# Kernel optimization log

Hardware: AMD Instinct MI355X
Metric: run time of the kernel (lower is better)

Reference implementation:

```python
import jax, jax.numpy as jnp
import numpy as np

T, B, E = 2048, 2, 1024
H = 16
D = E // H


def setup_inputs() -> dict:
    key = jax.random.key(0)
    ks = jax.random.split(key, 7)
    s = 1.0 / np.sqrt(E)
    return {
        "query": jax.random.normal(ks[0], (T, B, E), jnp.float32),
        "key": jax.random.normal(ks[1], (T, B, E), jnp.float32),
        "value": jax.random.normal(ks[2], (T, B, E), jnp.float32),
        "in_proj_weight": jax.random.normal(ks[3], (3 * E, E), jnp.float32) * s,
        "in_proj_bias": jax.random.normal(ks[4], (3 * E,), jnp.float32) * 0.02,
        "out_proj_weight": jax.random.normal(ks[5], (E, E), jnp.float32) * s,
        "out_proj_bias": jax.random.normal(ks[6], (E,), jnp.float32) * 0.02,
    }


def reference(query, key, value, in_proj_weight, in_proj_bias, out_proj_weight, out_proj_bias):
    tgt_len, bsz, embed_dim = query.shape
    src_len = key.shape[0]
    head_dim = embed_dim // H
    # packed in-projection (F.linear: x @ W.T + b)
    w_q, w_k, w_v = jnp.split(in_proj_weight, 3, axis=0)
    b_q, b_k, b_v = jnp.split(in_proj_bias, 3, axis=0)
    q = query @ w_q.T + b_q   # [T, B, E]
    k = key @ w_k.T + b_k     # [S, B, E]
    v = value @ w_v.T + b_v   # [S, B, E]
    # [T,B,E] -> [B,H,T,D]
    q = q.reshape(tgt_len, bsz, H, head_dim).transpose(1, 2, 0, 3)
    k = k.reshape(src_len, bsz, H, head_dim).transpose(1, 2, 0, 3)
    v = v.reshape(src_len, bsz, H, head_dim).transpose(1, 2, 0, 3)
    scale = 1.0 / jnp.sqrt(jnp.asarray(head_dim, q.dtype))
    scores = jnp.einsum("bhtd,bhsd->bhts", q, k) * scale  # [B,H,T,S]
    attn_weights = jax.nn.softmax(scores, axis=-1)
    attn = jnp.einsum("bhts,bhsd->bhtd", attn_weights, v)  # [B,H,T,D]
    # [B,H,T,D] -> [T,B,E]
    attn = attn.transpose(2, 0, 1, 3).reshape(tgt_len, bsz, embed_dim)
    attn_output = attn @ out_proj_weight.T + out_proj_bias  # [T,B,E]
    # averaged attention weights over heads (average_attn_weights=True)
    avg_weights = jnp.sum(attn_weights, axis=1) / H  # [B,T,S]
    return attn_output, avg_weights
```

## Files before the change

### kernel.cpp

```cpp
#include <hip/hip_runtime.h>
#include <hip/hip_bf16.h>

typedef float  f32x2  __attribute__((ext_vector_type(2)));
typedef float  f32x4  __attribute__((ext_vector_type(4)));
typedef float  f32x16 __attribute__((ext_vector_type(16)));
typedef __bf16 bf16x8 __attribute__((ext_vector_type(8)));

#define MFMA16(A,B,C) __builtin_amdgcn_mfma_f32_16x16x32_bf16((A),(B),(C),0,0,0)
#define MFMA32(A,B,C) __builtin_amdgcn_mfma_f32_32x32x16_bf16((A),(B),(C),0,0,0)
#define EXP2(x) __builtin_amdgcn_exp2f(x)
#define LOG2(x) __builtin_amdgcn_logf(x)

static constexpr int Tn = 2048, Bn = 2, En = 1024, Hn = 16, Dn = 64;
static constexpr float kQScale = 0.125f * 1.4426950408889634f;

static __device__ __forceinline__ unsigned pack2(float a, float b) {
  union { __bf16 h[2]; unsigned u; } un;
  un.h[0] = (__bf16)a; un.h[1] = (__bf16)b;
  return un.u;
}

static __device__ __forceinline__ void gload_lds16(const void* g, void* l) {
  __builtin_amdgcn_global_load_lds(
      (const __attribute__((address_space(1))) void*)g,
      (__attribute__((address_space(3))) void*)l, 16, 0, 0);
}

__global__ __launch_bounds__(256)
void k_cvt(const float* __restrict__ q, const float* __restrict__ k,
           const float* __restrict__ v, const float* __restrict__ w3,
           const float* __restrict__ wo,
           __bf16* __restrict__ qb, __bf16* __restrict__ kb,
           __bf16* __restrict__ vb, __bf16* __restrict__ w3b,
           __bf16* __restrict__ wob)
{
  const size_t g = (size_t)blockIdx.x * 256 + threadIdx.x;
  const float* src;
  __bf16* dst;
  size_t off;
  if (g < 524288)        { src = q;  dst = qb;  off = g; }
  else if (g < 1048576)  { src = k;  dst = kb;  off = g - 524288; }
  else if (g < 1572864)  { src = v;  dst = vb;  off = g - 1048576; }
  else if (g < 1966080)  { src = w3; dst = w3b; off = g - 1572864; }
  else                   { src = wo; dst = wob; off = g - 1966080; }
  const float* p = src + off * 8;
  f32x4 a = *reinterpret_cast<const f32x4*>(p);
  f32x4 b = *reinterpret_cast<const f32x4*>(p + 4);
  bf16x8 o;
  #pragma unroll
  for (int e = 0; e < 4; ++e) { o[e] = (__bf16)a[e]; o[e + 4] = (__bf16)b[e]; }
  *reinterpret_cast<bf16x8*>(dst + off * 8) = o;
}

__global__ __launch_bounds__(256)
void k_qkv(const __bf16* __restrict__ Xq, const __bf16* __restrict__ Xk,
           const __bf16* __restrict__ Xv, const __bf16* __restrict__ W,
           const float* __restrict__ bias,
           __bf16* __restrict__ q_ws, __bf16* __restrict__ k_ws,
           __bf16* __restrict__ v_ws)
{
  __shared__ __align__(16) char a_lds[2][8192];
  __shared__ __align__(16) char b_lds[2][8192];
  const int tid = threadIdx.x;
  const int lane = tid & 63, w = tid >> 6;
  const int wr = w >> 1, wc = w & 1;
  const int ag = lane >> 4, lr = lane & 15;
  const int mBase = blockIdx.x * 128;
  const int oBase = blockIdx.y * 128;
  const int which = blockIdx.y >> 3;
  const __bf16* X  = (which == 0) ? Xq : ((which == 1) ? Xk : Xv);
  const __bf16* Wt = W + (size_t)oBase * En;
  __bf16* dst = (which == 0) ? q_ws : ((which == 1) ? k_ws : v_ws);
  const float oscale = (which == 0) ? kQScale : 1.0f;

  const int gA = w;
  const __bf16* pa0 = X  + (size_t)(mBase + lane) * En + gA * 8;
  const __bf16* pa1 = X  + (size_t)(mBase + 64 + lane) * En + gA * 8;
  const __bf16* pb0 = Wt + (size_t)(lane) * En + gA * 8;
  const __bf16* pb1 = Wt + (size_t)(64 + lane) * En + gA * 8;

  f32x4 acc[4][4];
  #pragma unroll
  for (int i = 0; i < 4; ++i)
    #pragma unroll
    for (int j = 0; j < 4; ++j) { f32x4 z = {0.f, 0.f, 0.f, 0.f}; acc[i][j] = z; }

  gload_lds16(pa0, &a_lds[0][gA * 2048]);
  gload_lds16(pa1, &a_lds[0][gA * 2048 + 1024]);
  gload_lds16(pb0, &b_lds[0][gA * 2048]);
  gload_lds16(pb1, &b_lds[0][gA * 2048 + 1024]);
  __syncthreads();

  for (int kt = 0; kt < 32; ++kt) {
    const int cur = kt & 1, nxt = cur ^ 1;
    if (kt + 1 < 32) {
      const int kk = (kt + 1) * 32;
      gload_lds16(pa0 + kk, &a_lds[nxt][gA * 2048]);
      gload_lds16(pa1 + kk, &a_lds[nxt][gA * 2048 + 1024]);
      gload_lds16(pb0 + kk, &b_lds[nxt][gA * 2048]);
      gload_lds16(pb1 + kk, &b_lds[nxt][gA * 2048 + 1024]);
    }
    bf16x8 af[4], bfr[4];
    #pragma unroll
    for (int mb = 0; mb < 4; ++mb)
      af[mb] = *(const bf16x8*)(&a_lds[cur][ag * 2048 + (wr * 64 + mb * 16 + lr) * 16]);
    #pragma unroll
    for (int nb = 0; nb < 4; ++nb)
      bfr[nb] = *(const bf16x8*)(&b_lds[cur][ag * 2048 + (wc * 64 + nb * 16 + lr) * 16]);
    #pragma unroll
    for (int mb = 0; mb < 4; ++mb)
      #pragma unroll
      for (int nb = 0; nb < 4; ++nb)
        acc[mb][nb] = MFMA16(af[mb], bfr[nb], acc[mb][nb]);
    __syncthreads();
  }

  #pragma unroll
  for (int nb = 0; nb < 4; ++nb) {
    int oG = oBase + wc * 64 + nb * 16 + lr;
    float bv = bias[oG];
    int oS = oG & (En - 1);
    int h = oS >> 6, d = oS & 63;
    #pragma unroll
    for (int mb = 0; mb < 4; ++mb)
      #pragma unroll
      for (int r = 0; r < 4; ++r) {
        int i = mBase + wr * 64 + mb * 16 + ag * 4 + r;
        int t = i >> 1, b2 = i & 1;
        dst[(((size_t)(b2 * Hn + h)) * Tn + t) * Dn + d] =
            (__bf16)((acc[mb][nb][r] + bv) * oscale);
      }
  }
}

__global__ __launch_bounds__(256)
void k_transpose_v(const __bf16* __restrict__ v_ws, __bf16* __restrict__ vt_ws)
{
  __shared__ __bf16 tile[64][72];
  const int bh = blockIdx.x >> 5;
  const int tt = blockIdx.x & 31;
  const int tid = threadIdx.x;
  const __bf16* src = v_ws + ((size_t)bh * Tn + tt * 64) * Dn;
  #pragma unroll
  for (int it = 0; it < 2; ++it) {
    int gi = tid + it * 256;
    int row = gi >> 3, gg = gi & 7;
    *reinterpret_cast<bf16x8*>(&tile[row][gg * 8]) =
        *reinterpret_cast<const bf16x8*>(src + row * Dn + gg * 8);
  }
  __syncthreads();
  __bf16* dst = vt_ws + (size_t)bh * Dn * Tn + tt * 64;
  #pragma unroll
  for (int it = 0; it < 2; ++it) {
    int gi = tid + it * 256;
    int drow = gi >> 3, tg = gi & 7;
    bf16x8 vv;
    #pragma unroll
    for (int e = 0; e < 8; ++e) vv[e] = tile[tg * 8 + e][drow];
    *reinterpret_cast<bf16x8*>(dst + (size_t)drow * Tn + tg * 8) = vv;
  }
}

__global__ __launch_bounds__(256, 2)
void k_flash(const __bf16* __restrict__ q_ws, const __bf16* __restrict__ k_ws,
             const __bf16* __restrict__ vt_ws, __bf16* __restrict__ ctx,
             float* __restrict__ adj_g)
{
  __shared__ __align__(16) char kv_sm[2 * 16384];

  const int tid = threadIdx.x;
  const int lane = tid & 63, w = tid >> 6;
  const int tl = lane & 31, hi = lane >> 5;
  const int bh = blockIdx.x >> 4;
  const int qt = blockIdx.x & 15;
  const int t0w = qt * 128 + w * 32;

  const __bf16* kbase  = k_ws + (size_t)bh * Tn * Dn;
  const __bf16* vtbase = vt_ws + (size_t)bh * Dn * Tn;

  bf16x8 qf[4];
  {
    const __bf16* qrow = q_ws + ((size_t)bh * Tn + t0w + tl) * Dn + hi * 8;
    #pragma unroll
    for (int c = 0; c < 4; ++c)
      qf[c] = *reinterpret_cast<const bf16x8*>(qrow + c * 16);
  }

  union { unsigned u[4]; bf16x8 v; } onu;
  #pragma unroll
  for (int j = 0; j < 4; ++j) onu.u[j] = 0x3F803F80u;
  const bf16x8 kOne = onu.v;

  f32x16 accO0, accO1, accL;
  #pragma unroll
  for (int i = 0; i < 16; ++i) { accO0[i] = 0.f; accO1[i] = 0.f; accL[i] = 0.f; }
  float m_run = -INFINITY;

  const int r0 = tid >> 3, s0 = tid & 7;
  const int ldso = ((s0 ^ (r0 & 7)) << 4);
  const int ko0 = r0 * 128 + ldso;

  bf16x8 rk0 = *(const bf16x8*)(kbase + r0 * 64 + s0 * 8);
  bf16x8 rk1 = *(const bf16x8*)(kbase + (r0 + 32) * 64 + s0 * 8);
  bf16x8 rv0 = *(const bf16x8*)(vtbase + (size_t)r0 * Tn + s0 * 8);
  bf16x8 rv1 = *(const bf16x8*)(vtbase + (size_t)(r0 + 32) * Tn + s0 * 8);
  *(bf16x8*)(kv_sm + ko0) = rk0;
  *(bf16x8*)(kv_sm + ko0 + 4096) = rk1;
  *(bf16x8*)(kv_sm + 8192 + ko0) = rv0;
  *(bf16x8*)(kv_sm + 8192 + ko0 + 4096) = rv1;

  for (int st = 0; st < 32; ++st) {
    __syncthreads();
    const char* cur = kv_sm + (st & 1) * 16384;
    char* nxt = kv_sm + ((st + 1) & 1) * 16384;
    if (st + 1 < 32) {
      const __bf16* kn = kbase + (size_t)(st + 1) * 64 * Dn;
      const __bf16* vn = vtbase + (st + 1) * 64;
      rk0 = *(const bf16x8*)(kn + r0 * 64 + s0 * 8);
      rk1 = *(const bf16x8*)(kn + (r0 + 32) * 64 + s0 * 8);
      rv0 = *(const bf16x8*)(vn + (size_t)r0 * Tn + s0 * 8);
      rv1 = *(const bf16x8*)(vn + (size_t)(r0 + 32) * Tn + s0 * 8);
    }

    f32x16 sc0, sc1;
    #pragma unroll
    for (int i = 0; i < 16; ++i) { sc0[i] = 0.f; sc1[i] = 0.f; }
    const char* kr0 = cur + tl * 128;
    const char* kr1 = cur + (32 + tl) * 128;
    __builtin_amdgcn_s_setprio(1);
    #pragma unroll
    for (int c = 0; c < 4; ++c) {
      const int off = (((2 * c + hi) ^ (tl & 7)) << 4);
      sc0 = MFMA32(*(const bf16x8*)(kr0 + off), qf[c], sc0);
      sc1 = MFMA32(*(const bf16x8*)(kr1 + off), qf[c], sc1);
    }
    __builtin_amdgcn_s_setprio(0);

    float mx[8];
    #pragma unroll
    for (int i = 0; i < 8; ++i)
      mx[i] = fmaxf(fmaxf(sc0[i], sc0[i + 8]), fmaxf(sc1[i], sc1[i + 8]));
    float tm = fmaxf(fmaxf(fmaxf(mx[0], mx[1]), fmaxf(mx[2], mx[3])),
                     fmaxf(fmaxf(mx[4], mx[5]), fmaxf(mx[6], mx[7])));
    tm = fmaxf(tm, __shfl_xor(tm, 32, 64));
    if (__any(tm > m_run + 8.0f)) {
      const float mn = fmaxf(m_run, tm);
      const float es = EXP2(m_run - mn);
      m_run = mn;
      #pragma unroll
      for (int q = 0; q < 4; ++q)
        #pragma unroll
        for (int rr = 0; rr < 4; ++rr) {
          const float e = __shfl(es, 8 * q + 4 * hi + rr, 32);
          accO0[q * 4 + rr] *= e;
          accO1[q * 4 + rr] *= e;
          accL[q * 4 + rr] *= e;
        }
    }
    #pragma unroll
    for (int i = 0; i < 16; ++i) {
      sc0[i] = EXP2(sc0[i] - m_run);
      sc1[i] = EXP2(sc1[i] - m_run);
    }

    unsigned wA0[4], wB0[4], wA1[4], wB1[4];
    #pragma unroll
    for (int g = 0; g < 4; ++g) {
      wA0[g] = pack2(sc0[4 * g],     sc0[4 * g + 1]);
      wB0[g] = pack2(sc0[4 * g + 2], sc0[4 * g + 3]);
      wA1[g] = pack2(sc1[4 * g],     sc1[4 * g + 1]);
      wB1[g] = pack2(sc1[4 * g + 2], sc1[4 * g + 3]);
    }
    bf16x8 pa[2][2];
    #pragma unroll
    for (int sb = 0; sb < 2; ++sb) {
      const unsigned* WA = sb ? wA1 : wA0;
      const unsigned* WB = sb ? wB1 : wB0;
      #pragma unroll
      for (int c = 0; c < 2; ++c) {
        unsigned w0 = WA[2 * c], w2 = WA[2 * c + 1];
        unsigned w1 = WB[2 * c], w3 = WB[2 * c + 1];
        asm("v_permlane32_swap_b32 %0, %1" : "+v"(w0), "+v"(w2));
        asm("v_permlane32_swap_b32 %0, %1" : "+v"(w1), "+v"(w3));
        union { unsigned u[4]; bf16x8 v; } uu;
        uu.u[0] = w0; uu.u[1] = w1; uu.u[2] = w2; uu.u[3] = w3;
        pa[sb][c] = uu.v;
      }
    }

    const char* vr0 = cur + 8192 + tl * 128;
    const char* vr1 = cur + 8192 + (32 + tl) * 128;
    __builtin_amdgcn_s_setprio(1);
    #pragma unroll
    for (int sb = 0; sb < 2; ++sb)
      #pragma unroll
      for (int c = 0; c < 2; ++c) {
        const int off = (((sb * 4 + c * 2 + hi) ^ (tl & 7)) << 4);
        accO0 = MFMA32(pa[sb][c], *(const bf16x8*)(vr0 + off), accO0);
        accO1 = MFMA32(pa[sb][c], *(const bf16x8*)(vr1 + off), accO1);
        accL  = MFMA32(pa[sb][c], kOne, accL);
      }
    __builtin_amdgcn_s_setprio(0);

    if (st + 1 < 32) {
      *(bf16x8*)(nxt + ko0) = rk0;
      *(bf16x8*)(nxt + ko0 + 4096) = rk1;
      *(bf16x8*)(nxt + 8192 + ko0) = rv0;
      *(bf16x8*)(nxt + 8192 + ko0 + 4096) = rv1;
    }
  }

  const int b2 = bh >> 4, h = bh & 15;
  float adjv[16];
  #pragma unroll
  for (int q = 0; q < 4; ++q)
    #pragma unroll
    for (int rr = 0; rr < 4; ++rr) {
      const int j = q * 4 + rr;
      const float lv = 1.0f / accL[j];
      const int t = t0w + 8 * q + 4 * hi + rr;
      __bf16* cp = ctx + ((size_t)t * Bn + b2) * En + h * 64 + tl;
      cp[0]  = (__bf16)(accO0[j] * lv);
      cp[32] = (__bf16)(accO1[j] * lv);
      const float mrow = __shfl(m_run, 8 * q + 4 * hi + rr, 32);
      adjv[j] = mrow + LOG2(16.0f * accL[j]);
    }
  if (tl == 0) {
    #pragma unroll
    for (int q = 0; q < 4; ++q)
      #pragma unroll
      for (int rr = 0; rr < 4; ++rr) {
        const int t = t0w + 8 * q + 4 * hi + rr;
        adj_g[(size_t)bh * Tn + t] = adjv[q * 4 + rr];
      }
  }
}

__global__ __launch_bounds__(256)
void k_avgw(const __bf16* __restrict__ q_ws, const __bf16* __restrict__ k_ws,
            const float* __restrict__ adj_g, float* __restrict__ avg_out)
{
  __shared__ __align__(16) char q_sm[2][8192];
  __shared__ __align__(16) char k_sm[2][8192];
  __shared__ __align__(16) float adj_sm[16][64];

  const int tid = threadIdx.x;
  const int lane = tid & 63, w = tid >> 6;
  const int tl = lane & 31, hi = lane >> 5;
  const int b2 = blockIdx.x >> 10;
  const int tt = (blockIdx.x >> 5) & 31;
  const int ss = blockIdx.x & 31;
  const int thalf = (w >> 1) * 32, shalf = (w & 1) * 32;

  #pragma unroll
  for (int it = 0; it < 4; ++it) {
    int idx = tid + it * 256;
    int h = idx >> 6, trow = idx & 63;
    adj_sm[h][trow] = adj_g[((size_t)(b2 * Hn + h)) * Tn + tt * 64 + trow];
  }

  const size_t hstride = (size_t)Tn * Dn;
  const __bf16* qb = q_ws + ((size_t)(b2 * Hn) * Tn + tt * 64) * Dn;
  const __bf16* kb = k_ws + ((size_t)(b2 * Hn) * Tn + ss * 64) * Dn;

  const int r0 = tid >> 3, s0 = tid & 7;
  const int ldso = ((s0 ^ (r0 & 7)) << 4);
  const int ko0 = r0 * 128 + ldso;

  bf16x8 rq0 = *(const bf16x8*)(qb + r0 * 64 + s0 * 8);
  bf16x8 rq1 = *(const bf16x8*)(qb + (r0 + 32) * 64 + s0 * 8);
  bf16x8 rk0 = *(const bf16x8*)(kb + r0 * 64 + s0 * 8);
  bf16x8 rk1 = *(const bf16x8*)(kb + (r0 + 32) * 64 + s0 * 8);
  *(bf16x8*)(q_sm[0] + ko0) = rq0;
  *(bf16x8*)(q_sm[0] + ko0 + 4096) = rq1;
  *(bf16x8*)(k_sm[0] + ko0) = rk0;
  *(bf16x8*)(k_sm[0] + ko0 + 4096) = rk1;

  f32x16 avg;
  #pragma unroll
  for (int i = 0; i < 16; ++i) avg[i] = 0.f;

  for (int h = 0; h < Hn; ++h) {
    __syncthreads();
    const char* qc = q_sm[h & 1];
    const char* kc = k_sm[h & 1];
    char* qn = q_sm[(h + 1) & 1];
    char* kn = k_sm[(h + 1) & 1];
    if (h + 1 < Hn) {
      const __bf16* qp = qb + (size_t)(h + 1) * hstride;
      const __bf16* kp = kb + (size_t)(h + 1) * hstride;
      rq0 = *(const bf16x8*)(qp + r0 * 64 + s0 * 8);
      rq1 = *(const bf16x8*)(qp + (r0 + 32) * 64 + s0 * 8);
      rk0 = *(const bf16x8*)(kp + r0 * 64 + s0 * 8);
      rk1 = *(const bf16x8*)(kp + (r0 + 32) * 64 + s0 * 8);
    }

    f32x16 sc;
    #pragma unroll
    for (int i = 0; i < 16; ++i) sc[i] = 0.f;
    const char* qr = qc + (thalf + tl) * 128;
    const char* kr = kc + (shalf + tl) * 128;
    #pragma unroll
    for (int c = 0; c < 4; ++c) {
      const int off = (((2 * c + hi) ^ (tl & 7)) << 4);
      sc = MFMA32(*(const bf16x8*)(qr + off), *(const bf16x8*)(kr + off), sc);
    }

    #pragma unroll
    for (int q = 0; q < 4; ++q) {
      f32x4 ad = *(const f32x4*)&adj_sm[h][thalf + 8 * q + 4 * hi];
      #pragma unroll
      for (int r = 0; r < 4; ++r)
        avg[q * 4 + r] += EXP2(sc[q * 4 + r] - ad[r]);
    }

    if (h + 1 < Hn) {
      *(bf16x8*)(qn + ko0) = rq0;
      *(bf16x8*)(qn + ko0 + 4096) = rq1;
      *(bf16x8*)(kn + ko0) = rk0;
      *(bf16x8*)(kn + ko0 + 4096) = rk1;
    }
  }

  #pragma unroll
  for (int q = 0; q < 4; ++q)
    #pragma unroll
    for (int r = 0; r < 4; ++r) {
      int t = tt * 64 + thalf + 8 * q + 4 * hi + r;
      int s = ss * 64 + shalf + tl;
      avg_out[((size_t)(b2 * Tn + t)) * Tn + s] = avg[q * 4 + r];
    }
}

__global__ __launch_bounds__(256)
void k_outproj(const __bf16* __restrict__ ctx, const __bf16* __restrict__ W,
               const float* __restrict__ bias, float* __restrict__ out)
{
  __shared__ __align__(16) char a_lds[2][8192];
  __shared__ __align__(16) char b_lds[2][8192];
  const int tid = threadIdx.x;
  const int lane = tid & 63, w = tid >> 6;
  const int wr = w >> 1, wc = w & 1;
  const int ag = lane >> 4, lr = lane & 15;
  const int mBase = blockIdx.x * 128;
  const int oBase = blockIdx.y * 128;
  const __bf16* Wt = W + (size_t)oBase * En;

  const int gA = w;
  const __bf16* pa0 = ctx + (size_t)(mBase + lane) * En + gA * 8;
  const __bf16* pa1 = ctx + (size_t)(mBase + 64 + lane) * En + gA * 8;
  const __bf16* pb0 = Wt + (size_t)(lane) * En + gA * 8;
  const __bf16* pb1 = Wt + (size_t)(64 + lane) * En + gA * 8;

  f32x4 acc[4][4];
  #pragma unroll
  for (int i = 0; i < 4; ++i)
    #pragma unroll
    for (int j = 0; j < 4; ++j) { f32x4 z = {0.f,0.f,0.f,0.f}; acc[i][j] = z; }

  gload_lds16(pa0, &a_lds[0][gA * 2048]);
  gload_lds16(pa1, &a_lds[0][gA * 2048 + 1024]);
  gload_lds16(pb0, &b_lds[0][gA * 2048]);
  gload_lds16(pb1, &b_lds[0][gA * 2048 + 1024]);
  __syncthreads();

  for (int kt = 0; kt < 32; ++kt) {
    const int cur = kt & 1, nxt = cur ^ 1;
    if (kt + 1 < 32) {
      const int kk = (kt + 1) * 32;
      gload_lds16(pa0 + kk, &a_lds[nxt][gA * 2048]);
      gload_lds16(pa1 + kk, &a_lds[nxt][gA * 2048 + 1024]);
      gload_lds16(pb0 + kk, &b_lds[nxt][gA * 2048]);
      gload_lds16(pb1 + kk, &b_lds[nxt][gA * 2048 + 1024]);
    }
    bf16x8 af[4], bfr[4];
    #pragma unroll
    for (int mb = 0; mb < 4; ++mb)
      af[mb] = *(const bf16x8*)(&a_lds[cur][ag * 2048 + (wr * 64 + mb * 16 + lr) * 16]);
    #pragma unroll
    for (int nb = 0; nb < 4; ++nb)
      bfr[nb] = *(const bf16x8*)(&b_lds[cur][ag * 2048 + (wc * 64 + nb * 16 + lr) * 16]);
    #pragma unroll
    for (int mb = 0; mb < 4; ++mb)
      #pragma unroll
      for (int nb = 0; nb < 4; ++nb)
        acc[mb][nb] = MFMA16(af[mb], bfr[nb], acc[mb][nb]);
    __syncthreads();
  }

  #pragma unroll
  for (int nb = 0; nb < 4; ++nb) {
    int o = oBase + wc * 64 + nb * 16 + lr;
    float bv = bias[o];
    #pragma unroll
    for (int mb = 0; mb < 4; ++mb)
      #pragma unroll
      for (int r = 0; r < 4; ++r) {
        int i = mBase + wr * 64 + mb * 16 + ag * 4 + r;
        out[(size_t)i * En + o] = acc[mb][nb][r] + bv;
      }
  }
}

extern "C" void kernel_launch(void* const* d_in, const int* in_sizes, int n_in,
                              void* d_out, int out_size, void* d_ws, size_t ws_size,
                              hipStream_t stream)
{
  (void)in_sizes; (void)n_in; (void)out_size; (void)ws_size;
  const float* query = (const float*)d_in[0];
  const float* key   = (const float*)d_in[1];
  const float* value = (const float*)d_in[2];
  const float* in_w  = (const float*)d_in[3];
  const float* in_b  = (const float*)d_in[4];
  const float* out_w = (const float*)d_in[5];
  const float* out_b = (const float*)d_in[6];

  float* attn_out = (float*)d_out;
  float* avg_out  = (float*)d_out + (size_t)Tn * Bn * En;

  char* ws = (char*)d_ws;
  const size_t MB = 1u << 20;
  __bf16* q_ws  = (__bf16*)(ws);
  __bf16* k_ws  = (__bf16*)(ws + 8 * MB);
  __bf16* v_ws  = (__bf16*)(ws + 16 * MB);
  __bf16* vt_ws = (__bf16*)(ws + 24 * MB);
  __bf16* ctx   = (__bf16*)(ws + 32 * MB);
  float*  adj_g = (float*)(ws + 40 * MB);
  __bf16* xq_bf = vt_ws;
  __bf16* xk_bf = ctx;
  __bf16* xv_bf = (__bf16*)(ws + 40 * MB + 512 * 1024);
  __bf16* w3_bf = (__bf16*)(ws + 48 * MB + 512 * 1024);
  __bf16* wo_bf = (__bf16*)(ws + 54 * MB + 512 * 1024);

  k_cvt<<<8192, 256, 0, stream>>>(query, key, value, in_w, out_w,
                                  xq_bf, xk_bf, xv_bf, w3_bf, wo_bf);
  k_qkv<<<dim3(32, 24), 256, 0, stream>>>(xq_bf, xk_bf, xv_bf, w3_bf, in_b,
                                          q_ws, k_ws, v_ws);
  k_transpose_v<<<1024, 256, 0, stream>>>(v_ws, vt_ws);
  k_flash<<<512, 256, 0, stream>>>(q_ws, k_ws, vt_ws, ctx, adj_g);
  k_avgw<<<2048, 256, 0, stream>>>(q_ws, k_ws, adj_g, avg_out);
  k_outproj<<<dim3(32, 8), 256, 0, stream>>>(ctx, wo_bf, out_b, attn_out);
}
```

Baseline: 201.2 us.

## Restructure flash kernel to single-wave blocks loading K/V directly into registers

The flash attention kernel switches from 256-thread blocks sharing a double-buffered LDS tile of K/V to 64-thread single-wave blocks that load their MFMA fragments straight from global memory into registers. The loads are software-pipelined across two fragment sets, and the key step shrinks from 64 to 32 keys. This removes LDS stores, block-wide barriers and LDS reads. In exchange, each wave fetches K/V itself with no sharing across the four waves that previously reused one tile, so global or L2 traffic rises roughly fourfold and the launch grows to 2048 blocks.

```diff
diff --git a/kernel.cpp b/kernel.cpp
--- a/kernel.cpp
+++ b/kernel.cpp
@@ -161,26 +161,26 @@
   }
 }
 
-__global__ __launch_bounds__(256, 2)
+struct KvFrags { bf16x8 k[4]; bf16x8 v[4]; };
+
+__global__ __launch_bounds__(64, 2)
 void k_flash(const __bf16* __restrict__ q_ws, const __bf16* __restrict__ k_ws,
              const __bf16* __restrict__ vt_ws, __bf16* __restrict__ ctx,
              float* __restrict__ adj_g)
 {
-  __shared__ __align__(16) char kv_sm[2 * 16384];
-
   const int tid = threadIdx.x;
-  const int lane = tid & 63, w = tid >> 6;
-  const int tl = lane & 31, hi = lane >> 5;
-  const int bh = blockIdx.x >> 4;
-  const int qt = blockIdx.x & 15;
-  const int t0w = qt * 128 + w * 32;
-
-  const __bf16* kbase  = k_ws + (size_t)bh * Tn * Dn;
-  const __bf16* vtbase = vt_ws + (size_t)bh * Dn * Tn;
+  const int tl = tid & 31, hi = tid >> 5;
+  const int bh = blockIdx.x >> 6;
+  const int qt = blockIdx.x & 63;
+  const int t0 = qt * 32;
+
+  const __bf16* kp = k_ws + (size_t)bh * Tn * Dn + tl * 64 + hi * 8;
+  const __bf16* vp0 = vt_ws + (size_t)bh * Dn * Tn + (size_t)tl * Tn + hi * 8;
+  const __bf16* vp1 = vp0 + (size_t)32 * Tn;
 
   bf16x8 qf[4];
   {
-    const __bf16* qrow = q_ws + ((size_t)bh * Tn + t0w + tl) * Dn + hi * 8;
+    const __bf16* qrow = q_ws + ((size_t)bh * Tn + t0 + tl) * Dn + hi * 8;
     #pragma unroll
     for (int c = 0; c < 4; ++c)
       qf[c] = *reinterpret_cast<const bf16x8*>(qrow + c * 16);
@@ -196,143 +196,103 @@
   for (int i = 0; i < 16; ++i) { accO0[i] = 0.f; accO1[i] = 0.f; accL[i] = 0.f; }
   float m_run = -INFINITY;
 
-  const int r0 = tid >> 3, s0 = tid & 7;
-  const int ldso = ((s0 ^ (r0 & 7)) << 4);
-  const int ko0 = r0 * 128 + ldso;
-
-  bf16x8 rk0 = *(const bf16x8*)(kbase + r0 * 64 + s0 * 8);
-  bf16x8 rk1 = *(const bf16x8*)(kbase + (r0 + 32) * 64 + s0 * 8);
-  bf16x8 rv0 = *(const bf16x8*)(vtbase + (size_t)r0 * Tn + s0 * 8);
-  bf16x8 rv1 = *(const bf16x8*)(vtbase + (size_t)(r0 + 32) * Tn + s0 * 8);
-  *(bf16x8*)(kv_sm + ko0) = rk0;
-  *(bf16x8*)(kv_sm + ko0 + 4096) = rk1;
-  *(bf16x8*)(kv_sm + 8192 + ko0) = rv0;
-  *(bf16x8*)(kv_sm + 8192 + ko0 + 4096) = rv1;
-
-  for (int st = 0; st < 32; ++st) {
-    __syncthreads();
-    const char* cur = kv_sm + (st & 1) * 16384;
-    char* nxt = kv_sm + ((st + 1) & 1) * 16384;
-    if (st + 1 < 32) {
-      const __bf16* kn = kbase + (size_t)(st + 1) * 64 * Dn;
-      const __bf16* vn = vtbase + (st + 1) * 64;
-      rk0 = *(const bf16x8*)(kn + r0 * 64 + s0 * 8);
-      rk1 = *(const bf16x8*)(kn + (r0 + 32) * 64 + s0 * 8);
-      rv0 = *(const bf16x8*)(vn + (size_t)r0 * Tn + s0 * 8);
-      rv1 = *(const bf16x8*)(vn + (size_t)(r0 + 32) * Tn + s0 * 8);
-    }
-
-    f32x16 sc0, sc1;
-    #pragma unroll
-    for (int i = 0; i < 16; ++i) { sc0[i] = 0.f; sc1[i] = 0.f; }
-    const char* kr0 = cur + tl * 128;
-    const char* kr1 = cur + (32 + tl) * 128;
-    __builtin_amdgcn_s_setprio(1);
-    #pragma unroll
-    for (int c = 0; c < 4; ++c) {
-      const int off = (((2 * c + hi) ^ (tl & 7)) << 4);
-      sc0 = MFMA32(*(const bf16x8*)(kr0 + off), qf[c], sc0);
-      sc1 = MFMA32(*(const bf16x8*)(kr1 + off), qf[c], sc1);
-    }
-    __builtin_amdgcn_s_setprio(0);
-
-    float mx[8];
-    #pragma unroll
-    for (int i = 0; i < 8; ++i)
-      mx[i] = fmaxf(fmaxf(sc0[i], sc0[i + 8]), fmaxf(sc1[i], sc1[i + 8]));
-    float tm = fmaxf(fmaxf(fmaxf(mx[0], mx[1]), fmaxf(mx[2], mx[3])),
-                     fmaxf(fmaxf(mx[4], mx[5]), fmaxf(mx[6], mx[7])));
-    tm = fmaxf(tm, __shfl_xor(tm, 32, 64));
-    if (__any(tm > m_run + 8.0f)) {
-      const float mn = fmaxf(m_run, tm);
-      const float es = EXP2(m_run - mn);
-      m_run = mn;
-      #pragma unroll
-      for (int q = 0; q < 4; ++q)
-        #pragma unroll
-        for (int rr = 0; rr < 4; ++rr) {
-          const float e = __shfl(es, 8 * q + 4 * hi + rr, 32);
-          accO0[q * 4 + rr] *= e;
-          accO1[q * 4 + rr] *= e;
-          accL[q * 4 + rr] *= e;
-        }
-    }
-    #pragma unroll
-    for (int i = 0; i < 16; ++i) {
-      sc0[i] = EXP2(sc0[i] - m_run);
-      sc1[i] = EXP2(sc1[i] - m_run);
-    }
-
-    unsigned wA0[4], wB0[4], wA1[4], wB1[4];
-    #pragma unroll
-    for (int g = 0; g < 4; ++g) {
-      wA0[g] = pack2(sc0[4 * g],     sc0[4 * g + 1]);
-      wB0[g] = pack2(sc0[4 * g + 2], sc0[4 * g + 3]);
-      wA1[g] = pack2(sc1[4 * g],     sc1[4 * g + 1]);
-      wB1[g] = pack2(sc1[4 * g + 2], sc1[4 * g + 3]);
-    }
-    bf16x8 pa[2][2];
-    #pragma unroll
-    for (int sb = 0; sb < 2; ++sb) {
-      const unsigned* WA = sb ? wA1 : wA0;
-      const unsigned* WB = sb ? wB1 : wB0;
-      #pragma unroll
-      for (int c = 0; c < 2; ++c) {
-        unsigned w0 = WA[2 * c], w2 = WA[2 * c + 1];
-        unsigned w1 = WB[2 * c], w3 = WB[2 * c + 1];
-        asm("v_permlane32_swap_b32 %0, %1" : "+v"(w0), "+v"(w2));
-        asm("v_permlane32_swap_b32 %0, %1" : "+v"(w1), "+v"(w3));
-        union { unsigned u[4]; bf16x8 v; } uu;
-        uu.u[0] = w0; uu.u[1] = w1; uu.u[2] = w2; uu.u[3] = w3;
-        pa[sb][c] = uu.v;
-      }
-    }
-
-    const char* vr0 = cur + 8192 + tl * 128;
-    const char* vr1 = cur + 8192 + (32 + tl) * 128;
-    __builtin_amdgcn_s_setprio(1);
-    #pragma unroll
-    for (int sb = 0; sb < 2; ++sb)
-      #pragma unroll
-      for (int c = 0; c < 2; ++c) {
-        const int off = (((sb * 4 + c * 2 + hi) ^ (tl & 7)) << 4);
-        accO0 = MFMA32(pa[sb][c], *(const bf16x8*)(vr0 + off), accO0);
-        accO1 = MFMA32(pa[sb][c], *(const bf16x8*)(vr1 + off), accO1);
-        accL  = MFMA32(pa[sb][c], kOne, accL);
-      }
-    __builtin_amdgcn_s_setprio(0);
-
-    if (st + 1 < 32) {
-      *(bf16x8*)(nxt + ko0) = rk0;
-      *(bf16x8*)(nxt + ko0 + 4096) = rk1;
-      *(bf16x8*)(nxt + 8192 + ko0) = rv0;
-      *(bf16x8*)(nxt + 8192 + ko0 + 4096) = rv1;
-    }
-  }
+#define LOADKV(F, ST) do {                                                   \
+    const __bf16* kpt = kp + (size_t)(ST) * 2048;                            \
+    F.k[0] = *(const bf16x8*)(kpt);                                          \
+    F.k[1] = *(const bf16x8*)(kpt + 16);                                     \
+    F.k[2] = *(const bf16x8*)(kpt + 32);                                     \
+    F.k[3] = *(const bf16x8*)(kpt + 48);                                     \
+    const __bf16* vpt0 = vp0 + (ST) * 32;                                    \
+    const __bf16* vpt1 = vp1 + (ST) * 32;                                    \
+    F.v[0] = *(const bf16x8*)(vpt0);                                         \
+    F.v[1] = *(const bf16x8*)(vpt0 + 16);                                    \
+    F.v[2] = *(const bf16x8*)(vpt1);                                         \
+    F.v[3] = *(const bf16x8*)(vpt1 + 16);                                    \
+  } while (0)
+
+#define STEP(F) do {                                                         \
+    f32x16 sc;                                                               \
+    _Pragma("unroll")                                                        \
+    for (int i = 0; i < 16; ++i) sc[i] = 0.f;                                \
+    __builtin_amdgcn_s_setprio(1);                                           \
+    _Pragma("unroll")                                                        \
+    for (int c = 0; c < 4; ++c) sc = MFMA32(F.k[c], qf[c], sc);              \
+    __builtin_amdgcn_s_setprio(0);                                           \
+    float tm = sc[0];                                                        \
+    _Pragma("unroll")                                                        \
+    for (int i = 1; i < 16; ++i) tm = fmaxf(tm, sc[i]);                      \
+    tm = fmaxf(tm, __shfl_xor(tm, 32, 64));                                  \
+    if (__any(tm > m_run + 8.0f)) {                                          \
+      const float mn = fmaxf(m_run, tm);                                     \
+      const float es = EXP2(m_run - mn);                                     \
+      m_run = mn;                                                            \
+      _Pragma("unroll")                                                      \
+      for (int r = 0; r < 16; ++r) {                                         \
+        const float e = __shfl(es, (r & 3) + 8 * (r >> 2) + 4 * hi, 32);     \
+        accO0[r] *= e; accO1[r] *= e; accL[r] *= e;                          \
+      }                                                                      \
+    }                                                                        \
+    _Pragma("unroll")                                                        \
+    for (int i = 0; i < 16; ++i) sc[i] = EXP2(sc[i] - m_run);                \
+    unsigned wA[4], wB[4];                                                   \
+    _Pragma("unroll")                                                        \
+    for (int g = 0; g < 4; ++g) {                                            \
+      wA[g] = pack2(sc[4 * g], sc[4 * g + 1]);                               \
+      wB[g] = pack2(sc[4 * g + 2], sc[4 * g + 3]);                           \
+    }                                                                        \
+    bf16x8 pa[2];                                                            \
+    _Pragma("unroll")                                                        \
+    for (int c = 0; c < 2; ++c) {                                            \
+      unsigned w0 = wA[2 * c], w2 = wA[2 * c + 1];                           \
+      unsigned w1 = wB[2 * c], w3 = wB[2 * c + 1];                           \
+      asm("v_permlane32_swap_b32 %0, %1" : "+v"(w0), "+v"(w2));              \
+      asm("v_permlane32_swap_b32 %0, %1" : "+v"(w1), "+v"(w3));              \
+      union { unsigned u[4]; bf16x8 v; } uu;                                 \
+      uu.u[0] = w0; uu.u[1] = w1; uu.u[2] = w2; uu.u[3] = w3;                \
+      pa[c] = uu.v;                                                          \
+    }                                                                        \
+    __builtin_amdgcn_s_setprio(1);                                           \
+    _Pragma("unroll")                                                        \
+    for (int c = 0; c < 2; ++c) {                                            \
+      accO0 = MFMA32(pa[c], F.v[c], accO0);                                  \
+      accO1 = MFMA32(pa[c], F.v[2 + c], accO1);                              \
+      accL  = MFMA32(pa[c], kOne, accL);                                     \
+    }                                                                        \
+    __builtin_amdgcn_s_setprio(0);                                           \
+  } while (0)
+
+  KvFrags fA, fB;
+  LOADKV(fA, 0);
+  for (int st = 0; st < 64; st += 2) {
+    const int s1 = (st + 1 < 64) ? st + 1 : 63;
+    const int s2 = (st + 2 < 64) ? st + 2 : 63;
+    LOADKV(fB, s1);
+    STEP(fA);
+    LOADKV(fA, s2);
+    STEP(fB);
+  }
+#undef LOADKV
+#undef STEP
 
   const int b2 = bh >> 4, h = bh & 15;
   float adjv[16];
   #pragma unroll
-  for (int q = 0; q < 4; ++q)
-    #pragma unroll
-    for (int rr = 0; rr < 4; ++rr) {
-      const int j = q * 4 + rr;
-      const float lv = 1.0f / accL[j];
-      const int t = t0w + 8 * q + 4 * hi + rr;
-      __bf16* cp = ctx + ((size_t)t * Bn + b2) * En + h * 64 + tl;
-      cp[0]  = (__bf16)(accO0[j] * lv);
-      cp[32] = (__bf16)(accO1[j] * lv);
-      const float mrow = __shfl(m_run, 8 * q + 4 * hi + rr, 32);
-      adjv[j] = mrow + LOG2(16.0f * accL[j]);
-    }
+  for (int r = 0; r < 16; ++r) {
+    const int tp = (r & 3) + 8 * (r >> 2) + 4 * hi;
+    const int t = t0 + tp;
+    const float linv = 1.0f / accL[r];
+    __bf16* cp = ctx + ((size_t)t * Bn + b2) * En + h * 64 + tl;
+    cp[0]  = (__bf16)(accO0[r] * linv);
+    cp[32] = (__bf16)(accO1[r] * linv);
+    const float mrow = __shfl(m_run, tp, 32);
+    adjv[r] = mrow + LOG2(16.0f * accL[r]);
+  }
   if (tl == 0) {
     #pragma unroll
-    for (int q = 0; q < 4; ++q)
-      #pragma unroll
-      for (int rr = 0; rr < 4; ++rr) {
-        const int t = t0w + 8 * q + 4 * hi + rr;
-        adj_g[(size_t)bh * Tn + t] = adjv[q * 4 + rr];
-      }
+    for (int r = 0; r < 16; ++r) {
+      const int t = t0 + (r & 3) + 8 * (r >> 2) + 4 * hi;
+      adj_g[(size_t)bh * Tn + t] = adjv[r];
+    }
   }
 }
 
@@ -388,11 +348,11 @@
     char* kn = k_sm[(h + 1) & 1];
     if (h + 1 < Hn) {
       const __bf16* qp = qb + (size_t)(h + 1) * hstride;
-      const __bf16* kp = kb + (size_t)(h + 1) * hstride;
+      const __bf16* kp2 = kb + (size_t)(h + 1) * hstride;
       rq0 = *(const bf16x8*)(qp + r0 * 64 + s0 * 8);
       rq1 = *(const bf16x8*)(qp + (r0 + 32) * 64 + s0 * 8);
-      rk0 = *(const bf16x8*)(kp + r0 * 64 + s0 * 8);
-      rk1 = *(const bf16x8*)(kp + (r0 + 32) * 64 + s0 * 8);
+      rk0 = *(const bf16x8*)(kp2 + r0 * 64 + s0 * 8);
+      rk1 = *(const bf16x8*)(kp2 + (r0 + 32) * 64 + s0 * 8);
     }
 
     f32x16 sc;
@@ -537,7 +497,7 @@
   k_qkv<<<dim3(32, 24), 256, 0, stream>>>(xq_bf, xk_bf, xv_bf, w3_bf, in_b,
                                           q_ws, k_ws, v_ws);
   k_transpose_v<<<1024, 256, 0, stream>>>(v_ws, vt_ws);
-  k_flash<<<512, 256, 0, stream>>>(q_ws, k_ws, vt_ws, ctx, adj_g);
+  k_flash<<<2048, 64, 0, stream>>>(q_ws, k_ws, vt_ws, ctx, adj_g);
   k_avgw<<<2048, 256, 0, stream>>>(q_ws, k_ws, adj_g, avg_out);
   k_outproj<<<dim3(32, 8), 256, 0, stream>>>(ctx, wo_bf, out_b, attn_out);
 }
```

Result: slower. 264.1 us (+31.3%).

## Fuse activation bf16 conversion into QKV GEMM, retile outproj, change LDS swizzle

Applied to the files above, without the earlier changes.

The QKV projection now loads fp32 activations straight into LDS and converts them to bf16 while building MFMA fragments, so the conversion kernel only handles weights. This removes a separate read/write pass over the three activation tensors, at the cost of doubling the A-tile LDS footprint and adding conversion work inside the GEMM inner loop. The output projection uses 128x64 tiles, which doubles the grid for better occupancy and balance. The LDS XOR swizzle in the flash and avg-weights kernels is also changed to mix in higher row bits to reduce bank conflicts.

```diff
diff --git a/kernel.cpp b/kernel.cpp
--- a/kernel.cpp
+++ b/kernel.cpp
@@ -14,6 +14,8 @@
 static constexpr int Tn = 2048, Bn = 2, En = 1024, Hn = 16, Dn = 64;
 static constexpr float kQScale = 0.125f * 1.4426950408889634f;
 
+#define FSWZ(r) (((r) & 7) ^ ((((r) >> 3) & 3) << 1))
+
 static __device__ __forceinline__ unsigned pack2(float a, float b) {
   union { __bf16 h[2]; unsigned u; } un;
   un.h[0] = (__bf16)a; un.h[1] = (__bf16)b;
@@ -27,22 +29,15 @@
 }
 
 __global__ __launch_bounds__(256)
-void k_cvt(const float* __restrict__ q, const float* __restrict__ k,
-           const float* __restrict__ v, const float* __restrict__ w3,
-           const float* __restrict__ wo,
-           __bf16* __restrict__ qb, __bf16* __restrict__ kb,
-           __bf16* __restrict__ vb, __bf16* __restrict__ w3b,
-           __bf16* __restrict__ wob)
+void k_cvtw(const float* __restrict__ w3, const float* __restrict__ wo,
+            __bf16* __restrict__ w3b, __bf16* __restrict__ wob)
 {
   const size_t g = (size_t)blockIdx.x * 256 + threadIdx.x;
   const float* src;
   __bf16* dst;
   size_t off;
-  if (g < 524288)        { src = q;  dst = qb;  off = g; }
-  else if (g < 1048576)  { src = k;  dst = kb;  off = g - 524288; }
-  else if (g < 1572864)  { src = v;  dst = vb;  off = g - 1048576; }
-  else if (g < 1966080)  { src = w3; dst = w3b; off = g - 1572864; }
-  else                   { src = wo; dst = wob; off = g - 1966080; }
+  if (g < 393216) { src = w3; dst = w3b; off = g; }
+  else            { src = wo; dst = wob; off = g - 393216; }
   const float* p = src + off * 8;
   f32x4 a = *reinterpret_cast<const f32x4*>(p);
   f32x4 b = *reinterpret_cast<const f32x4*>(p + 4);
@@ -53,13 +48,13 @@
 }
 
 __global__ __launch_bounds__(256)
-void k_qkv(const __bf16* __restrict__ Xq, const __bf16* __restrict__ Xk,
-           const __bf16* __restrict__ Xv, const __bf16* __restrict__ W,
+void k_qkv(const float* __restrict__ Xq, const float* __restrict__ Xk,
+           const float* __restrict__ Xv, const __bf16* __restrict__ W,
            const float* __restrict__ bias,
            __bf16* __restrict__ q_ws, __bf16* __restrict__ k_ws,
            __bf16* __restrict__ v_ws)
 {
-  __shared__ __align__(16) char a_lds[2][8192];
+  __shared__ __align__(16) char a_lds[2][16384];
   __shared__ __align__(16) char b_lds[2][8192];
   const int tid = threadIdx.x;
   const int lane = tid & 63, w = tid >> 6;
@@ -68,16 +63,28 @@
   const int mBase = blockIdx.x * 128;
   const int oBase = blockIdx.y * 128;
   const int which = blockIdx.y >> 3;
-  const __bf16* X  = (which == 0) ? Xq : ((which == 1) ? Xk : Xv);
+  const float* X = (which == 0) ? Xq : ((which == 1) ? Xk : Xv);
   const __bf16* Wt = W + (size_t)oBase * En;
   __bf16* dst = (which == 0) ? q_ws : ((which == 1) ? k_ws : v_ws);
   const float oscale = (which == 0) ? kQScale : 1.0f;
 
-  const int gA = w;
-  const __bf16* pa0 = X  + (size_t)(mBase + lane) * En + gA * 8;
-  const __bf16* pa1 = X  + (size_t)(mBase + 64 + lane) * En + gA * 8;
-  const __bf16* pb0 = Wt + (size_t)(lane) * En + gA * 8;
-  const __bf16* pb1 = Wt + (size_t)(64 + lane) * En + gA * 8;
+  const int srow = (w & 1) * 64 + lane;
+  const int gw = w >> 1;
+  const float* paj[4];
+  const __bf16* pbj[2];
+  int aD[4], bD[2];
+  #pragma unroll
+  for (int j = 0; j < 4; ++j) {
+    const int g = 2 * j + gw;
+    paj[j] = X + (size_t)(mBase + srow) * En + g * 4;
+    aD[j] = g * 2048 + (w & 1) * 1024;
+  }
+  #pragma unroll
+  for (int j = 0; j < 2; ++j) {
+    const int g = 2 * j + gw;
+    pbj[j] = Wt + (size_t)srow * En + g * 8;
+    bD[j] = g * 2048 + (w & 1) * 1024;
+  }
 
   f32x4 acc[4][4];
   #pragma unroll
@@ -85,25 +92,32 @@
     #pragma unroll
     for (int j = 0; j < 4; ++j) { f32x4 z = {0.f, 0.f, 0.f, 0.f}; acc[i][j] = z; }
 
-  gload_lds16(pa0, &a_lds[0][gA * 2048]);
-  gload_lds16(pa1, &a_lds[0][gA * 2048 + 1024]);
-  gload_lds16(pb0, &b_lds[0][gA * 2048]);
-  gload_lds16(pb1, &b_lds[0][gA * 2048 + 1024]);
+  #pragma unroll
+  for (int j = 0; j < 4; ++j) gload_lds16(paj[j], &a_lds[0][aD[j]]);
+  #pragma unroll
+  for (int j = 0; j < 2; ++j) gload_lds16(pbj[j], &b_lds[0][bD[j]]);
   __syncthreads();
 
   for (int kt = 0; kt < 32; ++kt) {
     const int cur = kt & 1, nxt = cur ^ 1;
     if (kt + 1 < 32) {
       const int kk = (kt + 1) * 32;
-      gload_lds16(pa0 + kk, &a_lds[nxt][gA * 2048]);
-      gload_lds16(pa1 + kk, &a_lds[nxt][gA * 2048 + 1024]);
-      gload_lds16(pb0 + kk, &b_lds[nxt][gA * 2048]);
-      gload_lds16(pb1 + kk, &b_lds[nxt][gA * 2048 + 1024]);
+      #pragma unroll
+      for (int j = 0; j < 4; ++j) gload_lds16(paj[j] + kk, &a_lds[nxt][aD[j]]);
+      #pragma unroll
+      for (int j = 0; j < 2; ++j) gload_lds16(pbj[j] + kk, &b_lds[nxt][bD[j]]);
     }
     bf16x8 af[4], bfr[4];
     #pragma unroll
-    for (int mb = 0; mb < 4; ++mb)
-      af[mb] = *(const bf16x8*)(&a_lds[cur][ag * 2048 + (wr * 64 + mb * 16 + lr) * 16]);
+    for (int mb = 0; mb < 4; ++mb) {
+      const int row = wr * 64 + mb * 16 + lr;
+      f32x4 lo = *(const f32x4*)(&a_lds[cur][(2 * ag) * 2048 + row * 16]);
+      f32x4 hi = *(const f32x4*)(&a_lds[cur][(2 * ag + 1) * 2048 + row * 16]);
+      bf16x8 v;
+      #pragma unroll
+      for (int e = 0; e < 4; ++e) { v[e] = (__bf16)lo[e]; v[e + 4] = (__bf16)hi[e]; }
+      af[mb] = v;
+    }
     #pragma unroll
     for (int nb = 0; nb < 4; ++nb)
       bfr[nb] = *(const bf16x8*)(&b_lds[cur][ag * 2048 + (wc * 64 + nb * 16 + lr) * 16]);
@@ -197,8 +211,9 @@
   float m_run = -INFINITY;
 
   const int r0 = tid >> 3, s0 = tid & 7;
-  const int ldso = ((s0 ^ (r0 & 7)) << 4);
+  const int ldso = ((s0 ^ FSWZ(r0)) << 4);
   const int ko0 = r0 * 128 + ldso;
+  const int ftl = FSWZ(tl);
 
   bf16x8 rk0 = *(const bf16x8*)(kbase + r0 * 64 + s0 * 8);
   bf16x8 rk1 = *(const bf16x8*)(kbase + (r0 + 32) * 64 + s0 * 8);
@@ -230,7 +245,7 @@
     __builtin_amdgcn_s_setprio(1);
     #pragma unroll
     for (int c = 0; c < 4; ++c) {
-      const int off = (((2 * c + hi) ^ (tl & 7)) << 4);
+      const int off = (((2 * c + hi) ^ ftl) << 4);
       sc0 = MFMA32(*(const bf16x8*)(kr0 + off), qf[c], sc0);
       sc1 = MFMA32(*(const bf16x8*)(kr1 + off), qf[c], sc1);
     }
@@ -295,7 +310,7 @@
     for (int sb = 0; sb < 2; ++sb)
       #pragma unroll
       for (int c = 0; c < 2; ++c) {
-        const int off = (((sb * 4 + c * 2 + hi) ^ (tl & 7)) << 4);
+        const int off = (((sb * 4 + c * 2 + hi) ^ ftl) << 4);
         accO0 = MFMA32(pa[sb][c], *(const bf16x8*)(vr0 + off), accO0);
         accO1 = MFMA32(pa[sb][c], *(const bf16x8*)(vr1 + off), accO1);
         accL  = MFMA32(pa[sb][c], kOne, accL);
@@ -364,8 +379,9 @@
   const __bf16* kb = k_ws + ((size_t)(b2 * Hn) * Tn + ss * 64) * Dn;
 
   const int r0 = tid >> 3, s0 = tid & 7;
-  const int ldso = ((s0 ^ (r0 & 7)) << 4);
+  const int ldso = ((s0 ^ FSWZ(r0)) << 4);
   const int ko0 = r0 * 128 + ldso;
+  const int ftl = FSWZ(tl);
 
   bf16x8 rq0 = *(const bf16x8*)(qb + r0 * 64 + s0 * 8);
   bf16x8 rq1 = *(const bf16x8*)(qb + (r0 + 32) * 64 + s0 * 8);
@@ -388,11 +404,11 @@
     char* kn = k_sm[(h + 1) & 1];
     if (h + 1 < Hn) {
       const __bf16* qp = qb + (size_t)(h + 1) * hstride;
-      const __bf16* kp = kb + (size_t)(h + 1) * hstride;
+      const __bf16* kp2 = kb + (size_t)(h + 1) * hstride;
       rq0 = *(const bf16x8*)(qp + r0 * 64 + s0 * 8);
       rq1 = *(const bf16x8*)(qp + (r0 + 32) * 64 + s0 * 8);
-      rk0 = *(const bf16x8*)(kp + r0 * 64 + s0 * 8);
-      rk1 = *(const bf16x8*)(kp + (r0 + 32) * 64 + s0 * 8);
+      rk0 = *(const bf16x8*)(kp2 + r0 * 64 + s0 * 8);
+      rk1 = *(const bf16x8*)(kp2 + (r0 + 32) * 64 + s0 * 8);
     }
 
     f32x16 sc;
@@ -402,7 +418,7 @@
     const char* kr = kc + (shalf + tl) * 128;
     #pragma unroll
     for (int c = 0; c < 4; ++c) {
-      const int off = (((2 * c + hi) ^ (tl & 7)) << 4);
+      const int off = (((2 * c + hi) ^ ftl) << 4);
       sc = MFMA32(*(const bf16x8*)(qr + off), *(const bf16x8*)(kr + off), sc);
     }
 
@@ -437,51 +453,54 @@
                const float* __restrict__ bias, float* __restrict__ out)
 {
   __shared__ __align__(16) char a_lds[2][8192];
-  __shared__ __align__(16) char b_lds[2][8192];
+  __shared__ __align__(16) char b_lds[2][4096];
   const int tid = threadIdx.x;
   const int lane = tid & 63, w = tid >> 6;
-  const int wr = w >> 1, wc = w & 1;
   const int ag = lane >> 4, lr = lane & 15;
   const int mBase = blockIdx.x * 128;
-  const int oBase = blockIdx.y * 128;
-  const __bf16* Wt = W + (size_t)oBase * En;
-
-  const int gA = w;
-  const __bf16* pa0 = ctx + (size_t)(mBase + lane) * En + gA * 8;
-  const __bf16* pa1 = ctx + (size_t)(mBase + 64 + lane) * En + gA * 8;
-  const __bf16* pb0 = Wt + (size_t)(lane) * En + gA * 8;
-  const __bf16* pb1 = Wt + (size_t)(64 + lane) * En + gA * 8;
-
-  f32x4 acc[4][4];
-  #pragma unroll
-  for (int i = 0; i < 4; ++i)
+  const int oBase = blockIdx.y * 64;
+
+  const int srow = (w & 1) * 64 + lane;
+  const int gw = w >> 1;
+  const __bf16* paj[2];
+  int aD[2];
+  #pragma unroll
+  for (int j = 0; j < 2; ++j) {
+    const int g = 2 * j + gw;
+    paj[j] = ctx + (size_t)(mBase + srow) * En + g * 8;
+    aD[j] = g * 2048 + (w & 1) * 1024;
+  }
+  const __bf16* pb = W + (size_t)(oBase + lane) * En + w * 8;
+  const int bDst = w * 1024;
+
+  f32x4 acc[2][4];
+  #pragma unroll
+  for (int i = 0; i < 2; ++i)
     #pragma unroll
     for (int j = 0; j < 4; ++j) { f32x4 z = {0.f,0.f,0.f,0.f}; acc[i][j] = z; }
 
-  gload_lds16(pa0, &a_lds[0][gA * 2048]);
-  gload_lds16(pa1, &a_lds[0][gA * 2048 + 1024]);
-  gload_lds16(pb0, &b_lds[0][gA * 2048]);
-  gload_lds16(pb1, &b_lds[0][gA * 2048 + 1024]);
+  #pragma unroll
+  for (int j = 0; j < 2; ++j) gload_lds16(paj[j], &a_lds[0][aD[j]]);
+  gload_lds16(pb, &b_lds[0][bDst]);
   __syncthreads();
 
   for (int kt = 0; kt < 32; ++kt) {
     const int cur = kt & 1, nxt = cur ^ 1;
     if (kt + 1 < 32) {
       const int kk = (kt + 1) * 32;
-      gload_lds16(pa0 + kk, &a_lds[nxt][gA * 2048]);
-      gload_lds16(pa1 + kk, &a_lds[nxt][gA * 2048 + 1024]);
-      gload_lds16(pb0 + kk, &b_lds[nxt][gA * 2048]);
-      gload_lds16(pb1 + kk, &b_lds[nxt][gA * 2048 + 1024]);
-    }
-    bf16x8 af[4], bfr[4];
-    #pragma unroll
-    for (int mb = 0; mb < 4; ++mb)
-      af[mb] = *(const bf16x8*)(&a_lds[cur][ag * 2048 + (wr * 64 + mb * 16 + lr) * 16]);
+      #pragma unroll
+      for (int j = 0; j < 2; ++j) gload_lds16(paj[j] + kk, &a_lds[nxt][aD[j]]);
+      gload_lds16(pb + kk, &b_lds[nxt][bDst]);
+    }
+    bf16x8 af[2], bfr[4];
+    #pragma unroll
+    for (int mb = 0; mb < 2; ++mb)
+      af[mb] = *(const bf16x8*)(&a_lds[cur][ag * 2048 + (w * 32 + mb * 16 + lr) * 16]);
     #pragma unroll
     for (int nb = 0; nb < 4; ++nb)
-      bfr[nb] = *(const bf16x8*)(&b_lds[cur][ag * 2048 + (wc * 64 + nb * 16 + lr) * 16]);
-    #pragma unroll
-    for (int mb = 0; mb < 4; ++mb)
+      bfr[nb] = *(const bf16x8*)(&b_lds[cur][ag * 1024 + (nb * 16 + lr) * 16]);
+    #pragma unroll
+    for (int mb = 0; mb < 2; ++mb)
       #pragma unroll
       for (int nb = 0; nb < 4; ++nb)
         acc[mb][nb] = MFMA16(af[mb], bfr[nb], acc[mb][nb]);
@@ -490,13 +509,13 @@
 
   #pragma unroll
   for (int nb = 0; nb < 4; ++nb) {
-    int o = oBase + wc * 64 + nb * 16 + lr;
+    int o = oBase + nb * 16 + lr;
     float bv = bias[o];
     #pragma unroll
-    for (int mb = 0; mb < 4; ++mb)
+    for (int mb = 0; mb < 2; ++mb)
       #pragma unroll
       for (int r = 0; r < 4; ++r) {
-        int i = mBase + wr * 64 + mb * 16 + ag * 4 + r;
+        int i = mBase + w * 32 + mb * 16 + ag * 4 + r;
         out[(size_t)i * En + o] = acc[mb][nb][r] + bv;
       }
   }
@@ -526,18 +545,14 @@
   __bf16* vt_ws = (__bf16*)(ws + 24 * MB);
   __bf16* ctx   = (__bf16*)(ws + 32 * MB);
   float*  adj_g = (float*)(ws + 40 * MB);
-  __bf16* xq_bf = vt_ws;
-  __bf16* xk_bf = ctx;
-  __bf16* xv_bf = (__bf16*)(ws + 40 * MB + 512 * 1024);
-  __bf16* w3_bf = (__bf16*)(ws + 48 * MB + 512 * 1024);
-  __bf16* wo_bf = (__bf16*)(ws + 54 * MB + 512 * 1024);
-
-  k_cvt<<<8192, 256, 0, stream>>>(query, key, value, in_w, out_w,
-                                  xq_bf, xk_bf, xv_bf, w3_bf, wo_bf);
-  k_qkv<<<dim3(32, 24), 256, 0, stream>>>(xq_bf, xk_bf, xv_bf, w3_bf, in_b,
+  __bf16* w3_bf = (__bf16*)(ws + 41 * MB);
+  __bf16* wo_bf = (__bf16*)(ws + 47 * MB);
+
+  k_cvtw<<<2048, 256, 0, stream>>>(in_w, out_w, w3_bf, wo_bf);
+  k_qkv<<<dim3(32, 24), 256, 0, stream>>>(query, key, value, w3_bf, in_b,
                                           q_ws, k_ws, v_ws);
   k_transpose_v<<<1024, 256, 0, stream>>>(v_ws, vt_ws);
   k_flash<<<512, 256, 0, stream>>>(q_ws, k_ws, vt_ws, ctx, adj_g);
   k_avgw<<<2048, 256, 0, stream>>>(q_ws, k_ws, adj_g, avg_out);
-  k_outproj<<<dim3(32, 8), 256, 0, stream>>>(ctx, wo_bf, out_b, attn_out);
-}
+  k_outproj<<<dim3(32, 16), 256, 0, stream>>>(ctx, wo_bf, out_b, attn_out);
+}
```

After: 217.6 us. 8.2% more time.
